# Kernel tuning notes

Hardware: AMD Instinct MI355X
Metric: run time of the kernel (lower is better)

The kernel has to match this reference:

```python
import jax, jax.numpy as jnp
import numpy as np

B, T, D_IN, D_MODEL = 4, 4096, 256, 128


def setup_inputs() -> dict:
    key = jax.random.key(0)
    ks = jax.random.split(key, 7)
    s_in = 1.0 / np.sqrt(D_IN)
    return {
        "x": jax.random.normal(ks[0], (B, T, D_IN), dtype=jnp.float32),
        "Wq": jax.random.normal(ks[1], (D_IN, D_MODEL), dtype=jnp.float32) * s_in,
        "bq": jnp.zeros((D_MODEL,), dtype=jnp.float32),
        "Wk": jax.random.normal(ks[2], (D_IN, D_MODEL), dtype=jnp.float32) * s_in,
        "bk": jnp.zeros((D_MODEL,), dtype=jnp.float32),
        "Wv": jax.random.normal(ks[3], (D_IN, D_MODEL), dtype=jnp.float32) * s_in,
        "bv": jnp.zeros((D_MODEL,), dtype=jnp.float32),
    }


def reference(x, Wq, bq, Wk, bk, Wv, bv):
    # projections: (B,T,d_in) @ (d_in,d_model) -> (B,T,d_model)
    q = x @ Wq + bq
    k = x @ Wk + bk
    v = x @ Wv + bv
    # scores: (B,T,T), scaled by sqrt(d_model)
    scores = jnp.einsum("btd,bsd->bts", q, k) / np.sqrt(D_MODEL).astype(np.float32)
    attn = jax.nn.softmax(scores, axis=-1)
    out = jnp.einsum("bts,bsd->btd", attn, v)
    return out, attn
```

## Files before the change

kernel.cpp:

```cpp
#include <hip/hip_runtime.h>
#include <hip/hip_bf16.h>
#include <stdint.h>

#define TT 4096
#define DM 128
#define DIN 256
#define NB 4

typedef __attribute__((ext_vector_type(4))) float f32x4;
typedef __attribute__((ext_vector_type(8))) short s16x8;
typedef __attribute__((ext_vector_type(4))) short s16x4;

__device__ __forceinline__ unsigned short f2bf(float f) {
    union { float f; unsigned int u; } v; v.f = f;
    return (unsigned short)((v.u + 0x7FFFu + ((v.u >> 16) & 1u)) >> 16);
}
__device__ __forceinline__ float bf2f(unsigned short h) {
    union { unsigned int u; float f; } v; v.u = ((unsigned int)h) << 16;
    return v.f;
}

__device__ __forceinline__ void cp16(const void* g, void* l) {
    __builtin_amdgcn_global_load_lds(
        (__attribute__((address_space(1))) unsigned int*)(size_t)g,
        (__attribute__((address_space(3))) unsigned int*)l, 16, 0, 0);
}

__global__ __launch_bounds__(256) void k_wt(const float* __restrict__ Wq,
                                            const float* __restrict__ Wk,
                                            const float* __restrict__ Wv,
                                            unsigned short* __restrict__ Wtb) {
    int tid = blockIdx.x * 256 + threadIdx.x;
    int m = tid >> 15;
    int r = tid & 32767;
    int n = r >> 8;
    int k = r & 255;
    const float* W = (m == 0) ? Wq : (m == 1) ? Wk : Wv;
    Wtb[(size_t)tid] = f2bf(W[k * DM + n]);
}

__global__ __launch_bounds__(256) void k_proj(const float* __restrict__ x,
        const float* __restrict__ bq, const float* __restrict__ bk, const float* __restrict__ bv,
        const unsigned short* __restrict__ Wtb,
        unsigned short* __restrict__ Qb, unsigned short* __restrict__ Kb,
        unsigned short* __restrict__ Vb) {
    __shared__ __align__(16) unsigned short wt[DM][40];
    __shared__ __align__(16) unsigned short xl[64][40];
    int m = blockIdx.x >> 8;
    int tile = blockIdx.x & 255;
    int rowbase = tile * 64;
    int i = threadIdx.x;
    int w = i >> 6, l = i & 63;
    int lg = l >> 4, ll = l & 15;
    const float* bias = (m == 0) ? bq : (m == 1) ? bk : bv;
    unsigned short* out = (m == 0) ? Qb : (m == 1) ? Kb : Vb;
    const unsigned short* wsrc = Wtb + (size_t)m * DM * DIN;

    f32x4 acc[8];
    for (int n = 0; n < 8; n++) acc[n] = (f32x4){0.f, 0.f, 0.f, 0.f};

    for (int kk = 0; kk < 8; kk++) {
        int k0 = kk * 32;
        for (int t = 0; t < 2; t++) {
            int idx = i + t * 256;
            int row = idx >> 2, c8 = idx & 3;
            s16x8 v = *(const s16x8*)(wsrc + (size_t)row * DIN + k0 + c8 * 8);
            *(s16x8*)(&wt[row][c8 * 8]) = v;
        }
        for (int t = 0; t < 2; t++) {
            int idx = i + t * 256;
            int row = idx >> 3, c4 = idx & 7;
            f32x4 v = *(const f32x4*)(x + (size_t)(rowbase + row) * DIN + k0 + c4 * 4);
            s16x4 h;
            for (int j = 0; j < 4; j++) h[j] = (short)f2bf(v[j]);
            *(s16x4*)(&xl[row][c4 * 4]) = h;
        }
        __syncthreads();
        s16x8 a = *(const s16x8*)(&xl[w * 16 + ll][lg * 8]);
        for (int n = 0; n < 8; n++) {
            s16x8 b = *(const s16x8*)(&wt[n * 16 + ll][lg * 8]);
            acc[n] = __builtin_amdgcn_mfma_f32_16x16x32_bf16(a, b, acc[n], 0, 0, 0);
        }
        __syncthreads();
    }
    for (int n = 0; n < 8; n++) {
        int col = n * 16 + ll;
        float bv_ = bias[col];
        for (int j = 0; j < 4; j++) {
            int row = rowbase + w * 16 + lg * 4 + j;
            out[(size_t)row * DM + col] = f2bf(acc[n][j] + bv_);
        }
    }
}

__global__ __launch_bounds__(256) void k_vt(const unsigned short* __restrict__ Vb,
                                            unsigned short* __restrict__ Vtb) {
    __shared__ __align__(16) unsigned short tile[64][72];
    int bid = blockIdx.x;
    int b = bid >> 7;
    int rem = bid & 127;
    int tI = rem >> 1, dI = rem & 1;
    int t0 = tI * 64, d0 = dI * 64;
    int i = threadIdx.x;
    for (int t = 0; t < 2; t++) {
        int idx = i + t * 256;
        int r = idx >> 3, c8 = idx & 7;
        s16x8 v = *(const s16x8*)(Vb + ((size_t)(b * TT) + t0 + r) * DM + d0 + c8 * 8);
        *(s16x8*)(&tile[r][c8 * 8]) = v;
    }
    __syncthreads();
    for (int t = 0; t < 2; t++) {
        int idx = i + t * 256;
        int r2 = idx >> 3, c8 = idx & 7;
        s16x8 v;
        for (int j = 0; j < 8; j++) v[j] = (short)tile[c8 * 8 + j][r2];
        *(s16x8*)(Vtb + ((size_t)b * DM + d0 + r2) * TT + t0 + c8 * 8) = v;
    }
}

__global__ __launch_bounds__(512, 4) void k_attn(const unsigned short* __restrict__ Qb,
        const unsigned short* __restrict__ Kb, const unsigned short* __restrict__ Vtb,
        float* __restrict__ outO, float* __restrict__ outA) {
    __shared__ __align__(16) char smem[76288];

    int bid = blockIdx.x;
    int id2 = (bid & 7) * 64 + (bid >> 3);
    int b = id2 >> 7;
    int rowbase = (id2 & 127) * 32;
    int i = threadIdx.x;
    int w = i >> 6, l = i & 63;
    int rg = w & 1, ks = w >> 1;
    int lg = l >> 4, ll = l & 15;

    const unsigned short* Qrow = Qb + ((size_t)(b * TT) + rowbase) * DM;
    const unsigned short* Krow = Kb + (size_t)(b * TT) * DM;
    const unsigned short* Vt_b = Vtb + (size_t)b * DM * TT;
    const float scale = 0.08838834764831845f;

    unsigned short* Pw = (unsigned short*)(smem + 65536 + w * 1280);
    float* rsx = (float*)(smem + 75776);

    s16x8 qf[4];
    for (int c = 0; c < 4; c++)
        qf[c] = *(const s16x8*)(Qrow + (size_t)(rg * 16 + ll) * DM + c * 32 + lg * 8);

    int kr = ks * 16 + ll;

    auto stage_k = [&](char* kbuf, int s0) {
        for (int u = 0; u < 2; u++) {
            int c = u * 8 + w;
            int row = c * 4 + (l >> 4);
            int g = (l & 15) ^ (row & 7);
            cp16(Krow + (size_t)(s0 + row) * DM + g * 8, kbuf + c * 1024);
        }
    };
    auto stage_v = [&](char* vbuf, int s0) {
        for (int u = 0; u < 2; u++) {
            int c = u * 8 + w;
            int row = c * 8 + (l >> 3);
            int g = (l & 7) ^ (row & 7);
            cp16(Vt_b + (size_t)row * TT + s0 + g * 8, vbuf + c * 1024);
        }
    };
    auto qk = [&](const char* kbuf) -> f32x4 {
        const char* kbase = kbuf + kr * 256;
        f32x4 acc = (f32x4){0.f, 0.f, 0.f, 0.f};
        for (int c = 0; c < 4; c++) {
            s16x8 kf = *(const s16x8*)(kbase + (((c * 4 + lg) ^ (kr & 7)) << 4));
            acc = __builtin_amdgcn_mfma_f32_16x16x32_bf16(qf[c], kf, acc, 0, 0, 0);
        }
        return acc;
    };

    float rs[4] = {0.f, 0.f, 0.f, 0.f};
    stage_k(smem, 0);
    stage_k(smem + 16384, 64);
    stage_k(smem + 32768, 128);
    asm volatile("s_waitcnt vmcnt(4)" ::: "memory");
    __builtin_amdgcn_s_barrier();
    for (int t = 0; t < 64; t++) {
        if (t + 3 < 64) stage_k(smem + ((t + 3) & 3) * 16384, (t + 3) * 64);
        f32x4 acc = qk(smem + (t & 3) * 16384);
        for (int j = 0; j < 4; j++) rs[j] += __expf(acc[j] * scale);
        asm volatile("s_waitcnt vmcnt(4)" ::: "memory");
        __builtin_amdgcn_s_barrier();
    }
    asm volatile("s_waitcnt vmcnt(0)" ::: "memory");

    for (int mm = 1; mm < 16; mm <<= 1)
        for (int j = 0; j < 4; j++) rs[j] += __shfl_xor(rs[j], mm, 64);
    if (ll == 0)
        for (int j = 0; j < 4; j++) rsx[ks * 32 + rg * 16 + lg * 4 + j] = rs[j];
    __syncthreads();
    float inv_[4];
    for (int j = 0; j < 4; j++) {
        int row = rg * 16 + lg * 4 + j;
        inv_[j] = 1.0f / (rsx[row] + rsx[32 + row] + rsx[64 + row] + rsx[96 + row]);
    }

    for (int j = 0; j < 4; j++) Pw[(lg * 4 + j) * 40 + 16 + ll] = 0;
    f32x4 oacc[8];
    for (int n = 0; n < 8; n++) oacc[n] = (f32x4){0.f, 0.f, 0.f, 0.f};

    stage_k(smem, 0);
    stage_v(smem + 32768, 0);
    asm volatile("s_waitcnt vmcnt(0)" ::: "memory");
    __builtin_amdgcn_s_barrier();

    int cur = 0;
    for (int t = 0; t < 64; t++) {
        int s0 = t * 64;
        if (t < 63) {
            stage_k(smem + (cur ^ 1) * 16384, s0 + 64);
            stage_v(smem + 32768 + (cur ^ 1) * 16384, s0 + 64);
        }
        f32x4 acc = qk(smem + cur * 16384);
        for (int j = 0; j < 4; j++) {
            float p = __expf(acc[j] * scale) * inv_[j];
            Pw[(lg * 4 + j) * 40 + ll] = f2bf(p);
        }
        asm volatile("s_waitcnt lgkmcnt(0)" ::: "memory");
        __builtin_amdgcn_sched_barrier(0);
        s16x8 paf = *(const s16x8*)(Pw + ll * 40 + lg * 8);
        const char* vbuf = smem + 32768 + cur * 16384;
        for (int n8 = 0; n8 < 8; n8++) {
            int row = n8 * 16 + ll;
            int gl = ks * 2 + (lg & 1);
            s16x8 bfr = *(const s16x8*)(vbuf + row * 128 + ((gl ^ (row & 7)) << 4));
            oacc[n8] = __builtin_amdgcn_mfma_f32_16x16x32_bf16(paf, bfr, oacc[n8], 0, 0, 0);
        }
        {
            int arow = l >> 2, acol = (l & 3) * 4;
            s16x4 pv = *(const s16x4*)(Pw + arow * 40 + acol);
            f32x4 fv;
            for (int q = 0; q < 4; q++) fv[q] = bf2f((unsigned short)pv[q]);
            *(f32x4*)(outA + ((size_t)(b * TT) + rowbase + rg * 16 + arow) * TT
                      + s0 + ks * 16 + acol) = fv;
        }
        asm volatile("s_waitcnt vmcnt(1)" ::: "memory");
        __builtin_amdgcn_s_barrier();
        cur ^= 1;
    }

    float* obuf = (float*)smem;
    if (ks >= 1) {
        float* dst = obuf + (size_t)(rg * 3 + ks - 1) * 2112;
        for (int n8 = 0; n8 < 8; n8++)
            for (int j = 0; j < 4; j++)
                dst[(lg * 4 + j) * 132 + n8 * 16 + ll] = oacc[n8][j];
    }
    __syncthreads();
    if (ks == 0) {
        float* s1 = obuf + (size_t)(rg * 3 + 0) * 2112;
        float* s2 = obuf + (size_t)(rg * 3 + 1) * 2112;
        float* s3 = obuf + (size_t)(rg * 3 + 2) * 2112;
        for (int n8 = 0; n8 < 8; n8++)
            for (int j = 0; j < 4; j++) {
                int idx = (lg * 4 + j) * 132 + n8 * 16 + ll;
                s1[idx] = oacc[n8][j] + s1[idx] + s2[idx] + s3[idx];
            }
    }
    __syncthreads();
    {
        int row = i >> 4;
        int col = (i & 15) * 8;
        const float* src = obuf + (size_t)((row >> 4) * 3) * 2112 + (row & 15) * 132 + col;
        f32x4 v0 = *(const f32x4*)(src);
        f32x4 v1 = *(const f32x4*)(src + 4);
        float* dst = outO + ((size_t)(b * TT) + rowbase + row) * DM + col;
        *(f32x4*)dst = v0;
        *(f32x4*)(dst + 4) = v1;
    }
}

extern "C" void kernel_launch(void* const* d_in, const int* in_sizes, int n_in,
                              void* d_out, int out_size, void* d_ws, size_t ws_size,
                              hipStream_t stream) {
    const float* x  = (const float*)d_in[0];
    const float* Wq = (const float*)d_in[1];
    const float* bq = (const float*)d_in[2];
    const float* Wk = (const float*)d_in[3];
    const float* bk = (const float*)d_in[4];
    const float* Wv = (const float*)d_in[5];
    const float* bv = (const float*)d_in[6];
    float* outO = (float*)d_out;
    float* outA = outO + (size_t)NB * TT * DM;

    char* ws = (char*)d_ws;
    unsigned short* Qb  = (unsigned short*)(ws);
    unsigned short* Kb  = (unsigned short*)(ws + ((size_t)1 << 22));
    unsigned short* Vb  = (unsigned short*)(ws + ((size_t)2 << 22));
    unsigned short* Vtb = (unsigned short*)(ws + ((size_t)3 << 22));
    unsigned short* Wtb = (unsigned short*)(ws + ((size_t)4 << 22));

    k_wt<<<dim3(384), dim3(256), 0, stream>>>(Wq, Wk, Wv, Wtb);
    k_proj<<<dim3(768), dim3(256), 0, stream>>>(x, bq, bk, bv, Wtb, Qb, Kb, Vb);
    k_vt<<<dim3(512), dim3(256), 0, stream>>>(Vb, Vtb);
    k_attn<<<dim3(512), dim3(512), 0, stream>>>(Qb, Kb, Vtb, outO, outA);
}
```

Before: 147.6 us.

## Split softmax row-sum pass into separate wide kernel and shrink attention blocks

```diff
diff --git a/kernel.cpp b/kernel.cpp
--- a/kernel.cpp
+++ b/kernel.cpp
@@ -118,10 +118,85 @@
     }
 }
 
-__global__ __launch_bounds__(512, 4) void k_attn(const unsigned short* __restrict__ Qb,
+__global__ __launch_bounds__(256, 4) void k_rowsum(const unsigned short* __restrict__ Qb,
+        const unsigned short* __restrict__ Kb, float* __restrict__ rsum8) {
+    __shared__ __align__(16) char smem[24576];
+
+    int bid = blockIdx.x;
+    int id2 = (bid & 7) * 256 + (bid >> 3);
+    int b = id2 >> 9;
+    int rem = id2 & 511;
+    int rt = rem >> 2, kq = rem & 3;
+    int rowbase = rt * 32;
+    int i = threadIdx.x;
+    int w = i >> 6, l = i & 63;
+    int rg = w & 1, ks = w >> 1;
+    int lg = l >> 4, ll = l & 15;
+
+    const unsigned short* Qrow = Qb + ((size_t)(b * TT) + rowbase) * DM;
+    const unsigned short* Krow = Kb + (size_t)(b * TT) * DM + (size_t)(kq * 1024) * DM;
+    const float scale = 0.08838834764831845f;
+
+    s16x8 qf[4];
+    for (int c = 0; c < 4; c++)
+        qf[c] = *(const s16x8*)(Qrow + (size_t)(rg * 16 + ll) * DM + c * 32 + lg * 8);
+
+    int kr = ks * 16 + ll;
+    auto stage = [&](char* kbuf, int t) {
+        int s0 = t * 32;
+        for (int u = 0; u < 2; u++) {
+            int c = u * 4 + w;
+            int row = c * 4 + (l >> 4);
+            int g = (l & 15) ^ (row & 7);
+            cp16(Krow + (size_t)(s0 + row) * DM + g * 8, kbuf + c * 1024);
+        }
+    };
+
+    float rs[4] = {0.f, 0.f, 0.f, 0.f};
+    stage(smem, 0);
+    stage(smem + 8192, 1);
+    asm volatile("s_waitcnt vmcnt(2)" ::: "memory");
+    __builtin_amdgcn_s_barrier();
+
+    int cur = 0, nxt = 2;
+    for (int t = 0; t < 32; t++) {
+        int tn = (t + 2 <= 31) ? t + 2 : 31;
+        stage(smem + nxt * 8192, tn);
+        const char* kbase = smem + cur * 8192 + kr * 256;
+        f32x4 a0 = (f32x4){0.f, 0.f, 0.f, 0.f}, a1 = (f32x4){0.f, 0.f, 0.f, 0.f};
+        {
+            s16x8 k0 = *(const s16x8*)(kbase + (((0 * 4 + lg) ^ (kr & 7)) << 4));
+            s16x8 k1 = *(const s16x8*)(kbase + (((1 * 4 + lg) ^ (kr & 7)) << 4));
+            s16x8 k2 = *(const s16x8*)(kbase + (((2 * 4 + lg) ^ (kr & 7)) << 4));
+            s16x8 k3 = *(const s16x8*)(kbase + (((3 * 4 + lg) ^ (kr & 7)) << 4));
+            a0 = __builtin_amdgcn_mfma_f32_16x16x32_bf16(qf[0], k0, a0, 0, 0, 0);
+            a1 = __builtin_amdgcn_mfma_f32_16x16x32_bf16(qf[1], k1, a1, 0, 0, 0);
+            a0 = __builtin_amdgcn_mfma_f32_16x16x32_bf16(qf[2], k2, a0, 0, 0, 0);
+            a1 = __builtin_amdgcn_mfma_f32_16x16x32_bf16(qf[3], k3, a1, 0, 0, 0);
+        }
+        f32x4 acc;
+        for (int j = 0; j < 4; j++) acc[j] = a0[j] + a1[j];
+        for (int j = 0; j < 4; j++) rs[j] += __expf(acc[j] * scale);
+        asm volatile("s_waitcnt vmcnt(2)" ::: "memory");
+        __builtin_amdgcn_s_barrier();
+        cur++; if (cur == 3) cur = 0;
+        nxt++; if (nxt == 3) nxt = 0;
+    }
+    for (int mm = 1; mm < 16; mm <<= 1)
+        for (int j = 0; j < 4; j++) rs[j] += __shfl_xor(rs[j], mm, 64);
+    if (ll == 0) {
+        int p = kq * 2 + ks;
+        float* dst = rsum8 + ((size_t)(b * 8 + p)) * TT + rowbase + rg * 16 + lg * 4;
+        for (int j = 0; j < 4; j++) dst[j] = rs[j];
+    }
+}
+
+
+__global__ __launch_bounds__(256, 2) void k_attn(const unsigned short* __restrict__ Qb,
         const unsigned short* __restrict__ Kb, const unsigned short* __restrict__ Vtb,
+        const float* __restrict__ rsum8,
         float* __restrict__ outO, float* __restrict__ outA) {
-    __shared__ __align__(16) char smem[76288];
+    __shared__ __align__(16) char smem[70656];
 
     int bid = blockIdx.x;
     int id2 = (bid & 7) * 64 + (bid >> 3);
@@ -138,138 +213,118 @@
     const float scale = 0.08838834764831845f;
 
     unsigned short* Pw = (unsigned short*)(smem + 65536 + w * 1280);
-    float* rsx = (float*)(smem + 75776);
 
     s16x8 qf[4];
     for (int c = 0; c < 4; c++)
         qf[c] = *(const s16x8*)(Qrow + (size_t)(rg * 16 + ll) * DM + c * 32 + lg * 8);
 
+    float inv_[4];
+    for (int j = 0; j < 4; j++) {
+        int row = rowbase + rg * 16 + lg * 4 + j;
+        float s = 0.f;
+        for (int p = 0; p < 8; p++) s += rsum8[((size_t)(b * 8 + p)) * TT + row];
+        inv_[j] = 1.0f / s;
+    }
+
     int kr = ks * 16 + ll;
-
-    auto stage_k = [&](char* kbuf, int s0) {
+    auto stage = [&](char* slot, int t) {
+        int s0 = t * 32;
         for (int u = 0; u < 2; u++) {
-            int c = u * 8 + w;
+            int c = u * 4 + w;
             int row = c * 4 + (l >> 4);
             int g = (l & 15) ^ (row & 7);
-            cp16(Krow + (size_t)(s0 + row) * DM + g * 8, kbuf + c * 1024);
+            cp16(Krow + (size_t)(s0 + row) * DM + g * 8, slot + c * 1024);
+        }
+        for (int u = 0; u < 2; u++) {
+            int c = u * 4 + w;
+            int row = c * 16 + (l >> 2);
+            int g = (l & 3) ^ (row & 3);
+            cp16(Vt_b + (size_t)row * TT + s0 + g * 8, slot + 8192 + c * 1024);
         }
     };
-    auto stage_v = [&](char* vbuf, int s0) {
-        for (int u = 0; u < 2; u++) {
-            int c = u * 8 + w;
-            int row = c * 8 + (l >> 3);
-            int g = (l & 7) ^ (row & 7);
-            cp16(Vt_b + (size_t)row * TT + s0 + g * 8, vbuf + c * 1024);
-        }
-    };
-    auto qk = [&](const char* kbuf) -> f32x4 {
-        const char* kbase = kbuf + kr * 256;
-        f32x4 acc = (f32x4){0.f, 0.f, 0.f, 0.f};
-        for (int c = 0; c < 4; c++) {
-            s16x8 kf = *(const s16x8*)(kbase + (((c * 4 + lg) ^ (kr & 7)) << 4));
-            acc = __builtin_amdgcn_mfma_f32_16x16x32_bf16(qf[c], kf, acc, 0, 0, 0);
-        }
-        return acc;
-    };
-
-    float rs[4] = {0.f, 0.f, 0.f, 0.f};
-    stage_k(smem, 0);
-    stage_k(smem + 16384, 64);
-    stage_k(smem + 32768, 128);
-    asm volatile("s_waitcnt vmcnt(4)" ::: "memory");
-    __builtin_amdgcn_s_barrier();
-    for (int t = 0; t < 64; t++) {
-        if (t + 3 < 64) stage_k(smem + ((t + 3) & 3) * 16384, (t + 3) * 64);
-        f32x4 acc = qk(smem + (t & 3) * 16384);
-        for (int j = 0; j < 4; j++) rs[j] += __expf(acc[j] * scale);
-        asm volatile("s_waitcnt vmcnt(4)" ::: "memory");
-        __builtin_amdgcn_s_barrier();
-    }
-    asm volatile("s_waitcnt vmcnt(0)" ::: "memory");
-
-    for (int mm = 1; mm < 16; mm <<= 1)
-        for (int j = 0; j < 4; j++) rs[j] += __shfl_xor(rs[j], mm, 64);
-    if (ll == 0)
-        for (int j = 0; j < 4; j++) rsx[ks * 32 + rg * 16 + lg * 4 + j] = rs[j];
-    __syncthreads();
-    float inv_[4];
-    for (int j = 0; j < 4; j++) {
-        int row = rg * 16 + lg * 4 + j;
-        inv_[j] = 1.0f / (rsx[row] + rsx[32 + row] + rsx[64 + row] + rsx[96 + row]);
-    }
 
     for (int j = 0; j < 4; j++) Pw[(lg * 4 + j) * 40 + 16 + ll] = 0;
     f32x4 oacc[8];
     for (int n = 0; n < 8; n++) oacc[n] = (f32x4){0.f, 0.f, 0.f, 0.f};
 
-    stage_k(smem, 0);
-    stage_v(smem + 32768, 0);
-    asm volatile("s_waitcnt vmcnt(0)" ::: "memory");
+    stage(smem, 0);
+    stage(smem + 16384, 1);
+    stage(smem + 32768, 2);
+    asm volatile("s_waitcnt vmcnt(8)" ::: "memory");
     __builtin_amdgcn_s_barrier();
 
-    int cur = 0;
-    for (int t = 0; t < 64; t++) {
-        int s0 = t * 64;
-        if (t < 63) {
-            stage_k(smem + (cur ^ 1) * 16384, s0 + 64);
-            stage_v(smem + 32768 + (cur ^ 1) * 16384, s0 + 64);
-        }
-        f32x4 acc = qk(smem + cur * 16384);
+    for (int t = 0; t < 128; t++) {
+        int s0 = t * 32;
+        int tn = (t + 3 <= 127) ? t + 3 : 127;
+        stage(smem + ((t + 3) & 3) * 16384, tn);
+
+        const char* kbase = smem + (t & 3) * 16384 + kr * 256;
+        f32x4 a0 = (f32x4){0.f, 0.f, 0.f, 0.f}, a1 = (f32x4){0.f, 0.f, 0.f, 0.f};
+        {
+            s16x8 k0 = *(const s16x8*)(kbase + (((0 * 4 + lg) ^ (kr & 7)) << 4));
+            s16x8 k1 = *(const s16x8*)(kbase + (((1 * 4 + lg) ^ (kr & 7)) << 4));
+            s16x8 k2 = *(const s16x8*)(kbase + (((2 * 4 + lg) ^ (kr & 7)) << 4));
+            s16x8 k3 = *(const s16x8*)(kbase + (((3 * 4 + lg) ^ (kr & 7)) << 4));
+            a0 = __builtin_amdgcn_mfma_f32_16x16x32_bf16(qf[0], k0, a0, 0, 0, 0);
+            a1 = __builtin_amdgcn_mfma_f32_16x16x32_bf16(qf[1], k1, a1, 0, 0, 0);
+            a0 = __builtin_amdgcn_mfma_f32_16x16x32_bf16(qf[2], k2, a0, 0, 0, 0);
+            a1 = __builtin_amdgcn_mfma_f32_16x16x32_bf16(qf[3], k3, a1, 0, 0, 0);
+        }
         for (int j = 0; j < 4; j++) {
-            float p = __expf(acc[j] * scale) * inv_[j];
+            float p = __expf((a0[j] + a1[j]) * scale) * inv_[j];
             Pw[(lg * 4 + j) * 40 + ll] = f2bf(p);
         }
         asm volatile("s_waitcnt lgkmcnt(0)" ::: "memory");
         __builtin_amdgcn_sched_barrier(0);
-        s16x8 paf = *(const s16x8*)(Pw + ll * 40 + lg * 8);
-        const char* vbuf = smem + 32768 + cur * 16384;
-        for (int n8 = 0; n8 < 8; n8++) {
-            int row = n8 * 16 + ll;
+        {
+            s16x8 paf = *(const s16x8*)(Pw + ll * 40 + lg * 8);
+            const char* vbuf = smem + (t & 3) * 16384 + 8192;
             int gl = ks * 2 + (lg & 1);
-            s16x8 bfr = *(const s16x8*)(vbuf + row * 128 + ((gl ^ (row & 7)) << 4));
-            oacc[n8] = __builtin_amdgcn_mfma_f32_16x16x32_bf16(paf, bfr, oacc[n8], 0, 0, 0);
+            for (int n8 = 0; n8 < 8; n8++) {
+                int row = n8 * 16 + ll;
+                s16x8 bfr = *(const s16x8*)(vbuf + row * 64 + ((gl ^ (row & 3)) << 4));
+                oacc[n8] = __builtin_amdgcn_mfma_f32_16x16x32_bf16(paf, bfr, oacc[n8], 0, 0, 0);
+            }
         }
         {
             int arow = l >> 2, acol = (l & 3) * 4;
             s16x4 pv = *(const s16x4*)(Pw + arow * 40 + acol);
             f32x4 fv;
             for (int q = 0; q < 4; q++) fv[q] = bf2f((unsigned short)pv[q]);
-            *(f32x4*)(outA + ((size_t)(b * TT) + rowbase + rg * 16 + arow) * TT
-                      + s0 + ks * 16 + acol) = fv;
-        }
-        asm volatile("s_waitcnt vmcnt(1)" ::: "memory");
+            __builtin_nontemporal_store(fv,
+                (f32x4*)(outA + ((size_t)(b * TT) + rowbase + rg * 16 + arow) * TT
+                         + s0 + ks * 16 + acol));
+        }
+        asm volatile("s_waitcnt vmcnt(9)" ::: "memory");
         __builtin_amdgcn_s_barrier();
-        cur ^= 1;
-    }
-
+    }
+
+    asm volatile("s_waitcnt vmcnt(0)" ::: "memory");
+    __builtin_amdgcn_s_barrier();
     float* obuf = (float*)smem;
-    if (ks >= 1) {
-        float* dst = obuf + (size_t)(rg * 3 + ks - 1) * 2112;
+    if (ks == 1) {
+        float* dst = obuf + (size_t)rg * 2112;
         for (int n8 = 0; n8 < 8; n8++)
             for (int j = 0; j < 4; j++)
                 dst[(lg * 4 + j) * 132 + n8 * 16 + ll] = oacc[n8][j];
     }
     __syncthreads();
     if (ks == 0) {
-        float* s1 = obuf + (size_t)(rg * 3 + 0) * 2112;
-        float* s2 = obuf + (size_t)(rg * 3 + 1) * 2112;
-        float* s3 = obuf + (size_t)(rg * 3 + 2) * 2112;
+        float* dst = obuf + (size_t)rg * 2112;
         for (int n8 = 0; n8 < 8; n8++)
             for (int j = 0; j < 4; j++) {
                 int idx = (lg * 4 + j) * 132 + n8 * 16 + ll;
-                s1[idx] = oacc[n8][j] + s1[idx] + s2[idx] + s3[idx];
+                dst[idx] += oacc[n8][j];
             }
     }
     __syncthreads();
     {
-        int row = i >> 4;
-        int col = (i & 15) * 8;
-        const float* src = obuf + (size_t)((row >> 4) * 3) * 2112 + (row & 15) * 132 + col;
-        f32x4 v0 = *(const f32x4*)(src);
-        f32x4 v1 = *(const f32x4*)(src + 4);
-        float* dst = outO + ((size_t)(b * TT) + rowbase + row) * DM + col;
-        *(f32x4*)dst = v0;
-        *(f32x4*)(dst + 4) = v1;
+        int row = i >> 3;
+        int colf = (i & 7) * 16;
+        const float* src = obuf + (size_t)(row >> 4) * 2112 + (row & 15) * 132 + colf;
+        float* dst = outO + ((size_t)(b * TT) + rowbase + row) * DM + colf;
+        for (int u = 0; u < 4; u++)
+            *(f32x4*)(dst + u * 4) = *(const f32x4*)(src + u * 4);
     }
 }
 
@@ -292,9 +347,11 @@
     unsigned short* Vb  = (unsigned short*)(ws + ((size_t)2 << 22));
     unsigned short* Vtb = (unsigned short*)(ws + ((size_t)3 << 22));
     unsigned short* Wtb = (unsigned short*)(ws + ((size_t)4 << 22));
+    float* rsum8 = (float*)(ws + ((size_t)2 << 22));
 
     k_wt<<<dim3(384), dim3(256), 0, stream>>>(Wq, Wk, Wv, Wtb);
     k_proj<<<dim3(768), dim3(256), 0, stream>>>(x, bq, bk, bv, Wtb, Qb, Kb, Vb);
     k_vt<<<dim3(512), dim3(256), 0, stream>>>(Vb, Vtb);
-    k_attn<<<dim3(512), dim3(512), 0, stream>>>(Qb, Kb, Vtb, outO, outA);
-}
+    k_rowsum<<<dim3(2048), dim3(256), 0, stream>>>(Qb, Kb, rsum8);
+    k_attn<<<dim3(512), dim3(256), 0, stream>>>(Qb, Kb, Vtb, rsum8, outO, outA);
+}
```

Measured after the change: 157.2 us. +6.5%, slower.
